# Kernel tuning notes

Hardware: AMD Instinct MI355X
Metric: run time of the kernel (lower is better)

Reference implementation:

```python
import jax, jax.numpy as jnp
import numpy as np

B, L, H, D, VOC, C, P = 16, 256, 6, 768, 32000, 20, 1
d = D // H
MAXF = 20
BN_EPS = 1e-5


def setup_inputs() -> dict:
    key = jax.random.key(0)
    ks = jax.random.split(key, 8)
    doc_tids = jax.random.randint(ks[0], (B, L), 0, VOC)
    TFs = jax.random.uniform(ks[1], (B, L), dtype=jnp.float32) * 20.0 + 1.0
    DFs = jax.random.uniform(ks[2], (B, L), dtype=jnp.float32) * 1000.0 + 1.0
    emb = jax.random.normal(ks[3], (VOC, D), dtype=jnp.float32) * 0.02
    fcW = jax.random.normal(ks[4], (C + P, D), dtype=jnp.float32) * 0.02
    fcb = jnp.zeros((C + P,), dtype=jnp.float32)
    weiW = jax.random.normal(ks[5], (2, H), dtype=jnp.float32) * 0.1
    weib = jnp.zeros((2,), dtype=jnp.float32)
    return dict(doc_tids=doc_tids, TFs=TFs, DFs=DFs, emb=emb,
                fcW=fcW, fcb=fcb, weiW=weiW, weib=weib)


def _bn(x):
    # BatchNorm over channel axis 1 (H), batch stats over all other axes (train mode, affine=False)
    m = x.mean(axis=(0, 2, 3), keepdims=True)
    v = x.var(axis=(0, 2, 3), keepdims=True)
    return (x - m) * jax.lax.rsqrt(v + BN_EPS)


def _leaky9(x):
    return jnp.where(x >= 0, x, 9.0 * x)


def reference(doc_tids, TFs, DFs, emb, fcW, fcb, weiW, weib):
    # --- EmbbedingTFIDF (eval mode, dropout off): tf-idf weighted embedding lookup ---
    tf = jnp.minimum(TFs, float(MAXF))
    idf = jnp.log1p(1.0 / DFs)
    x = emb[doc_tids] * (tf * idf)[:, :, None]          # (B, L, D)
    valid = doc_tids != 0
    # model flips pad_mask with logical_not, then co_weights[pad_mask] = 0
    invalid = ~(valid[:, :, None] & valid[:, None, :])  # (B, L, L) True -> zero out
    mask = invalid[:, None, :, :]                       # broadcast over heads

    def split_heads(h):
        return h.reshape(B, L, H, d).transpose(0, 2, 1, 3)  # (B, H, L, d)

    Q = split_heads(x)
    K = Q
    V = Q

    # --- nearAttention (layers=1) ---
    Vn = _bn(V)
    # DistMatrix: pairwise Euclidean distance dist[b,h,i,j] = ||K_i - Q_j||
    Ksq = jnp.sum(K * K, axis=-1)[..., :, None]
    Qsq = jnp.sum(Q * Q, axis=-1)[..., None, :]
    cross = jnp.einsum('bhid,bhjd->bhij', K, Q)
    co = jnp.sqrt(jnp.maximum(Ksq + Qsq - 2.0 * cross, 1e-12))  # (B, H, L, L)
    # BatchNorm1d(H) over flattened (B, H, L*L) == per-H stats over (0,2,3)
    co = _leaky9(_bn(co))
    co = jnp.where(mask, 0.0, co)
    co = jax.nn.softmax(co, axis=-1)
    co = jnp.where(jnp.isnan(co), 0.0, co)
    V_out = jnp.einsum('bhij,bhjd->bhid', co, Vn)
    Q_out = _bn(jnp.einsum('bhij,bhjd->bhid', co, Q))
    K_out = _bn(jnp.einsum('bhij,bhjd->bhid', co, K))

    # --- head ---
    Vc = V_out.transpose(0, 2, 1, 3).reshape(B, L, D)       # catHiddens
    V_lgts = jax.nn.softmax(Vc @ fcW.T + fcb, axis=-1)      # (B, L, C+P)
    cw = jnp.swapaxes(co, -1, -2).reshape(B, L * L, H)      # transpose then contiguous reshape
    cw = jax.nn.softmax(cw @ weiW.T + weib, axis=-1)        # (B, L*L, 2)
    cw = cw.reshape(B, L, L, 2).sum(axis=-2, keepdims=True)[:, :, :, 0]  # (B, L, 1)
    cw = jax.nn.softmax(cw, axis=-1)                        # softmax over singleton -> ones (faithful)
    logits = (cw * V_lgts).sum(axis=1)[:, :C]               # (B, C)
    logits = jax.nn.softmax(logits, axis=-1)
    return logits
```

## Files before the change

kernel.cpp:

```cpp
#include <hip/hip_runtime.h>
#include <hip/hip_bf16.h>
#include <math.h>

#define OFF_XH   0UL
#define OFF_XT   1572864UL
#define OFF_VC   3145728UL
#define OFF_SQ   4718592UL
#define OFF_THS  4743168UL
#define OFF_PART 4767744UL
#define OFF_STAT 4780032UL
#define OFF_ACC  4780056UL
#define OFF_FCWB 4780392UL

typedef __attribute__((ext_vector_type(8))) __bf16 bf16x8;
typedef __attribute__((ext_vector_type(4))) float f32x4;
typedef __attribute__((ext_vector_type(8))) unsigned short u16x8;

__global__ __launch_bounds__(256) void k1_gather(const int* __restrict__ tids,
    const float* __restrict__ TF, const float* __restrict__ DF,
    const float* __restrict__ emb, unsigned short* __restrict__ xh,
    unsigned short* __restrict__ xT, float* __restrict__ sq, float* __restrict__ ths) {
  int bh = blockIdx.x >> 4, tg = blockIdx.x & 15;
  int b = bh / 6, h = bh % 6;
  int T0 = tg * 16;
  int tid = threadIdx.x;
  __shared__ float swgt[16];
  __shared__ int stid[16];
  __shared__ unsigned short tT[128][18];
  if (tid < 16) {
    int tok = b * 256 + T0 + tid;
    stid[tid] = tids[tok];
    swgt[tid] = fminf(TF[tok], 20.0f) * log1pf(1.0f / DF[tok]);
  }
  __syncthreads();
  int r = tid >> 4, c8 = (tid & 15) * 8;
  const float* er = emb + (size_t)stid[r] * 768 + h * 128 + c8;
  float wgt = swgt[r];
  float4 e0 = *(const float4*)er;
  float4 e1 = *(const float4*)(er + 4);
  float f[8] = {e0.x, e0.y, e0.z, e0.w, e1.x, e1.y, e1.z, e1.w};
  float s1 = 0.0f, s2 = 0.0f;
  u16x8 pk;
#pragma unroll
  for (int e = 0; e < 8; ++e) {
    __hip_bfloat16 hb = __float2bfloat16(f[e] * wgt);
    float g = __bfloat162float(hb);
    s1 += g; s2 += g * g;
    pk[e] = __bfloat16_as_ushort(hb);
  }
  *(u16x8*)(xh + ((size_t)(bh * 256 + T0 + r)) * 128 + c8) = pk;
  s1 += __shfl_down(s1, 8); s1 += __shfl_down(s1, 4);
  s1 += __shfl_down(s1, 2); s1 += __shfl_down(s1, 1);
  s2 += __shfl_down(s2, 8); s2 += __shfl_down(s2, 4);
  s2 += __shfl_down(s2, 2); s2 += __shfl_down(s2, 1);
  if ((tid & 15) == 0) {
    ths[bh * 256 + T0 + r] = s1;
    sq[bh * 256 + T0 + r]  = s2;
  }
#pragma unroll
  for (int j = 0; j < 8; ++j) tT[c8 + j][r] = pk[j];
  __syncthreads();
  int ch = tid >> 1, half = tid & 1;
  unsigned int* xo = (unsigned int*)xT + ((size_t)(bh * 128 + ch)) * 128 + tg * 8 + half * 4;
#pragma unroll
  for (int k = 0; k < 4; ++k)
    xo[k] = *(const unsigned int*)&tT[ch][(half * 4 + k) * 2];
}

__global__ __launch_bounds__(256) void k2_stats(const unsigned short* __restrict__ xh,
    const float* __restrict__ sq, float* __restrict__ part) {
  int p = blockIdx.x, bh = blockIdx.y;
  int tid = threadIdx.x, w = tid >> 6, lane = tid & 63;
  int quad = lane >> 4, l16 = lane & 15;
  int I = p * 16;
  const __bf16* xb = (const __bf16*)xh + (size_t)bh * 256 * 128;
  bf16x8 a[4];
#pragma unroll
  for (int k0 = 0; k0 < 4; ++k0)
    a[k0] = *(const bf16x8*)(xb + (size_t)(I + l16) * 128 + k0 * 32 + quad * 8);
  const float* sqh = sq + (size_t)bh * 256;
  float si[4];
#pragma unroll
  for (int r = 0; r < 4; ++r) si[r] = sqh[I + quad * 4 + r];
  float ls1 = 0.0f, ls2 = 0.0f;
#pragma unroll
  for (int tl = 0; tl < 4; ++tl) {
    int t = w * 4 + tl;
    f32x4 acc = {0.0f, 0.0f, 0.0f, 0.0f};
#pragma unroll
    for (int k0 = 0; k0 < 4; ++k0) {
      bf16x8 bfr = *(const bf16x8*)(xb + (size_t)(t * 16 + l16) * 128 + k0 * 32 + quad * 8);
      acc = __builtin_amdgcn_mfma_f32_16x16x32_bf16(a[k0], bfr, acc, 0, 0, 0);
    }
    float sj = sqh[t * 16 + l16];
#pragma unroll
    for (int r = 0; r < 4; ++r) {
      float cv = sqrtf(fmaxf(si[r] + sj - 2.0f * acc[r], 1e-12f));
      ls1 += cv; ls2 += cv * cv;
    }
  }
#pragma unroll
  for (int off = 32; off >= 1; off >>= 1) {
    ls1 += __shfl_down(ls1, off);
    ls2 += __shfl_down(ls2, off);
  }
  if (lane == 0) {
    part[(((size_t)bh * 16 + p) * 4 + w) * 2 + 0] = ls1;
    part[(((size_t)bh * 16 + p) * 4 + w) * 2 + 1] = ls2;
  }
}

__global__ __launch_bounds__(384) void k3_stats(const float* __restrict__ ths,
    const float* __restrict__ sq, const float* __restrict__ part,
    const float* __restrict__ fcW, float* __restrict__ stats,
    float* __restrict__ acc, unsigned short* __restrict__ fcWb) {
  int h = threadIdx.x >> 6, lane = threadIdx.x & 63;
  float s1 = 0.0f, s2 = 0.0f;
  for (int m = 0; m < 64; ++m) {
    int f = m * 64 + lane;
    int bb = f >> 8, l = f & 255;
    size_t idx = ((size_t)(bb * 6 + h)) * 256 + l;
    s1 += ths[idx]; s2 += sq[idx];
  }
#pragma unroll
  for (int off = 32; off >= 1; off >>= 1) {
    s1 += __shfl_down(s1, off);
    s2 += __shfl_down(s2, off);
  }
  if (lane == 0) {
    float cnt = 524288.0f;
    float mean = s1 / cnt;
    float var = s2 / cnt - mean * mean;
    stats[h] = mean;
    stats[6 + h] = rsqrtf(var + 1e-5f);
  }
  float c1 = 0.0f, c2 = 0.0f;
#pragma unroll
  for (int t = 0; t < 16; ++t) {
    int e = lane + 64 * t;
    int bb = e >> 6, rest = e & 63, pp = rest >> 2, ww = rest & 3;
    size_t pidx = ((((size_t)(bb * 6 + h)) * 16 + pp) * 4 + ww) * 2;
    c1 += part[pidx]; c2 += part[pidx + 1];
  }
#pragma unroll
  for (int off = 32; off >= 1; off >>= 1) {
    c1 += __shfl_down(c1, off);
    c2 += __shfl_down(c2, off);
  }
  if (lane == 0) {
    float cnt = 1048576.0f;
    float mean = c1 / cnt;
    float var = c2 / cnt - mean * mean;
    stats[12 + h] = mean;
    stats[18 + h] = rsqrtf(var + 1e-5f);
  }
  if (threadIdx.x < 336) acc[threadIdx.x] = 0.0f;
  for (int idx = threadIdx.x; idx < 21 * 768; idx += 384)
    fcWb[idx] = __bfloat16_as_ushort(__float2bfloat16(fcW[idx]));
}

__global__ __launch_bounds__(256, 4) void k45_fused(const unsigned short* __restrict__ xh,
    const unsigned short* __restrict__ xT, const int* __restrict__ tids,
    const float* __restrict__ sq, const float* __restrict__ stats,
    unsigned short* __restrict__ vc16) {
  int p = blockIdx.x, bh = blockIdx.y;
  int b = bh / 6, h = bh % 6;
  int tid = threadIdx.x, w = tid >> 6, lane = tid & 63;
  int quad = lane >> 4, l16 = lane & 15;
  int I = p * 16;
  __shared__ float svld[256];
  __shared__ float ssq[256];
  __shared__ unsigned short cot[16][264];
  __shared__ float smax[16][4];
  __shared__ float ssum[16][4];
  svld[tid] = (tids[b * 256 + tid] != 0) ? 1.0f : 0.0f;
  ssq[tid] = sq[(size_t)bh * 256 + tid];
  const __bf16* xb = (const __bf16*)xh + (size_t)bh * 256 * 128;
  bf16x8 a[4];
#pragma unroll
  for (int k0 = 0; k0 < 4; ++k0)
    a[k0] = *(const bf16x8*)(xb + (size_t)(I + l16) * 128 + k0 * 32 + quad * 8);
  __syncthreads();
  float m = stats[12 + h], rsc = stats[18 + h];
  float rv[4], si[4];
#pragma unroll
  for (int r = 0; r < 4; ++r) {
    rv[r] = svld[I + quad * 4 + r];
    si[r] = ssq[I + quad * 4 + r];
  }
  float y[4][4];
#pragma unroll
  for (int tl = 0; tl < 4; ++tl) {
    int t = w * 4 + tl;
    f32x4 acc = {0.0f, 0.0f, 0.0f, 0.0f};
#pragma unroll
    for (int k0 = 0; k0 < 4; ++k0) {
      bf16x8 bfr = *(const bf16x8*)(xb + (size_t)(t * 16 + l16) * 128 + k0 * 32 + quad * 8);
      acc = __builtin_amdgcn_mfma_f32_16x16x32_bf16(a[k0], bfr, acc, 0, 0, 0);
    }
    float sj = ssq[t * 16 + l16];
    float cvld = svld[t * 16 + l16];
#pragma unroll
    for (int r = 0; r < 4; ++r) {
      float cv = sqrtf(fmaxf(si[r] + sj - 2.0f * acc[r], 1e-12f));
      float yv = (cv - m) * rsc;
      yv = yv >= 0.0f ? yv : 9.0f * yv;
      y[tl][r] = yv * rv[r] * cvld;
    }
  }
#pragma unroll
  for (int r = 0; r < 4; ++r) {
    float mx = fmaxf(fmaxf(y[0][r], y[1][r]), fmaxf(y[2][r], y[3][r]));
#pragma unroll
    for (int off = 1; off <= 8; off <<= 1) mx = fmaxf(mx, __shfl_xor(mx, off));
    if (l16 == 0) smax[quad * 4 + r][w] = mx;
  }
  __syncthreads();
  float gmx[4];
#pragma unroll
  for (int r = 0; r < 4; ++r) {
    int row = quad * 4 + r;
    gmx[r] = fmaxf(fmaxf(smax[row][0], smax[row][1]), fmaxf(smax[row][2], smax[row][3]));
    float s = 0.0f;
#pragma unroll
    for (int tl = 0; tl < 4; ++tl) { y[tl][r] = expf(y[tl][r] - gmx[r]); s += y[tl][r]; }
#pragma unroll
    for (int off = 1; off <= 8; off <<= 1) s += __shfl_xor(s, off);
    if (l16 == 0) ssum[row][w] = s;
  }
  __syncthreads();
#pragma unroll
  for (int r = 0; r < 4; ++r) {
    int row = quad * 4 + r;
    float gs = ssum[row][0] + ssum[row][1] + ssum[row][2] + ssum[row][3];
    float inv = 1.0f / gs;
#pragma unroll
    for (int tl = 0; tl < 4; ++tl)
      cot[row][w * 64 + tl * 16 + l16] =
          __bfloat16_as_ushort(__float2bfloat16(y[tl][r] * inv));
  }
  __syncthreads();
  bf16x8 a2[8];
#pragma unroll
  for (int k0 = 0; k0 < 8; ++k0)
    a2[k0] = *(const bf16x8*)&cot[l16][k0 * 32 + quad * 8];
  const __bf16* xbT = (const __bf16*)xT + (size_t)bh * 128 * 256;
  float mv = stats[h], rvs = stats[6 + h];
  float rm = rvs * mv;
  size_t vbase = ((size_t)(b * 256 + I + quad * 4)) * 768 + h * 128;
#pragma unroll
  for (int jl = 0; jl < 2; ++jl) {
    int ch = (w * 2 + jl) * 16 + l16;
    const __bf16* brow = xbT + (size_t)ch * 256;
    f32x4 vacc = {0.0f, 0.0f, 0.0f, 0.0f};
#pragma unroll
    for (int k0 = 0; k0 < 8; ++k0) {
      bf16x8 bfr = *(const bf16x8*)(brow + k0 * 32 + quad * 8);
      vacc = __builtin_amdgcn_mfma_f32_16x16x32_bf16(a2[k0], bfr, vacc, 0, 0, 0);
    }
#pragma unroll
    for (int r = 0; r < 4; ++r) {
      float ov = rvs * vacc[r] - rm;
      vc16[vbase + (size_t)r * 768 + ch] = __bfloat16_as_ushort(__float2bfloat16(ov));
    }
  }
}

__global__ __launch_bounds__(256) void k5b_lgts(const unsigned short* __restrict__ vc16,
    const unsigned short* __restrict__ fcWb, const float* __restrict__ fcb,
    float* __restrict__ acc) {
  int b = blockIdx.x >> 2, qa = blockIdx.x & 3;
  int tid = threadIdx.x, w = tid >> 6, lane = tid & 63;
  int quad = lane >> 4, l16 = lane & 15;
  int tok0 = b * 256 + qa * 64 + w * 16;
  int c1c = (l16 < 5) ? (16 + l16) : 20;
  const __bf16* vb = (const __bf16*)vc16;
  const __bf16* w0 = (const __bf16*)fcWb + (size_t)l16 * 768;
  const __bf16* w1 = (const __bf16*)fcWb + (size_t)c1c * 768;
  f32x4 ac0 = {0.0f, 0.0f, 0.0f, 0.0f}, ac1 = {0.0f, 0.0f, 0.0f, 0.0f};
#pragma unroll
  for (int k0 = 0; k0 < 24; ++k0) {
    int ko = k0 * 32 + quad * 8;
    bf16x8 af = *(const bf16x8*)(vb + (size_t)(tok0 + l16) * 768 + ko);
    bf16x8 b0 = *(const bf16x8*)(w0 + ko);
    bf16x8 b1 = *(const bf16x8*)(w1 + ko);
    ac0 = __builtin_amdgcn_mfma_f32_16x16x32_bf16(af, b0, ac0, 0, 0, 0);
    ac1 = __builtin_amdgcn_mfma_f32_16x16x32_bf16(af, b1, ac1, 0, 0, 0);
  }
  float bias0 = fcb[l16];
  float bias1 = (l16 < 5) ? fcb[16 + l16] : 0.0f;
  float p0s = 0.0f, p1s = 0.0f;
#pragma unroll
  for (int r = 0; r < 4; ++r) {
    float lg0 = ac0[r] + bias0;
    float lg1 = (l16 < 5) ? (ac1[r] + bias1) : -1e30f;
    float mx = fmaxf(lg0, lg1);
#pragma unroll
    for (int off = 1; off <= 8; off <<= 1) mx = fmaxf(mx, __shfl_xor(mx, off));
    float e0 = expf(lg0 - mx), e1 = expf(lg1 - mx);
    float s = e0 + e1;
#pragma unroll
    for (int off = 1; off <= 8; off <<= 1) s += __shfl_xor(s, off);
    float inv = 1.0f / s;
    p0s += e0 * inv;
    p1s += e1 * inv;
  }
  p0s += __shfl_xor(p0s, 16); p0s += __shfl_xor(p0s, 32);
  p1s += __shfl_xor(p1s, 16); p1s += __shfl_xor(p1s, 32);
  __shared__ float sacc[4][21];
  if (quad == 0) sacc[w][l16] = p0s;
  if (quad == 1 && l16 < 5) sacc[w][16 + l16] = p1s;
  __syncthreads();
  if (tid < 21) {
    float s = sacc[0][tid] + sacc[1][tid] + sacc[2][tid] + sacc[3][tid];
    atomicAdd(&acc[b * 21 + tid], s);
  }
}

__global__ __launch_bounds__(64) void k6_final(const float* __restrict__ acc,
                                               float* __restrict__ out) {
  int b = threadIdx.x;
  if (b < 16) {
    float mx = -1e30f;
    for (int c = 0; c < 20; ++c) mx = fmaxf(mx, acc[b * 21 + c]);
    float e[20], s = 0.0f;
    for (int c = 0; c < 20; ++c) { e[c] = expf(acc[b * 21 + c] - mx); s += e[c]; }
    float inv = 1.0f / s;
    for (int c = 0; c < 20; ++c) out[b * 20 + c] = e[c] * inv;
  }
}

extern "C" void kernel_launch(void* const* d_in, const int* in_sizes, int n_in,
                              void* d_out, int out_size, void* d_ws, size_t ws_size,
                              hipStream_t stream) {
  const int*   tids = (const int*)d_in[0];
  const float* TF   = (const float*)d_in[1];
  const float* DF   = (const float*)d_in[2];
  const float* emb  = (const float*)d_in[3];
  const float* fcW  = (const float*)d_in[4];
  const float* fcb  = (const float*)d_in[5];
  float* out = (float*)d_out;
  float* ws  = (float*)d_ws;
  unsigned short* xh   = (unsigned short*)(ws + OFF_XH);
  unsigned short* xT   = (unsigned short*)(ws + OFF_XT);
  unsigned short* vc   = (unsigned short*)(ws + OFF_VC);
  unsigned short* fcWb = (unsigned short*)(ws + OFF_FCWB);
  float* sq    = ws + OFF_SQ;
  float* ths   = ws + OFF_THS;
  float* part  = ws + OFF_PART;
  float* stats = ws + OFF_STAT;
  float* acc   = ws + OFF_ACC;

  k1_gather<<<1536, 256, 0, stream>>>(tids, TF, DF, emb, xh, xT, sq, ths);
  k2_stats<<<dim3(16, 96), 256, 0, stream>>>(xh, sq, part);
  k3_stats<<<1, 384, 0, stream>>>(ths, sq, part, fcW, stats, acc, fcWb);
  k45_fused<<<dim3(16, 96), 256, 0, stream>>>(xh, xT, tids, sq, stats, vc);
  k5b_lgts<<<64, 256, 0, stream>>>(vc, fcWb, fcb, acc);
  k6_final<<<1, 64, 0, stream>>>(acc, out);
}
```

Baseline: 214.4 us.

## Fuse gather with distance-stats kernel via LDS tile and fold final softmax

Result: faster. 207.4 us (-3.3%).

```diff
diff --git a/kernel.cpp b/kernel.cpp
--- a/kernel.cpp
+++ b/kernel.cpp
@@ -10,93 +10,124 @@
 #define OFF_PART 4767744UL
 #define OFF_STAT 4780032UL
 #define OFF_ACC  4780056UL
-#define OFF_FCWB 4780392UL
+#define OFF_CTR  4780392UL
+#define OFF_FCWB 4780396UL
 
 typedef __attribute__((ext_vector_type(8))) __bf16 bf16x8;
 typedef __attribute__((ext_vector_type(4))) float f32x4;
 typedef __attribute__((ext_vector_type(8))) unsigned short u16x8;
 
-__global__ __launch_bounds__(256) void k1_gather(const int* __restrict__ tids,
+__global__ __launch_bounds__(512) void k12_fused(const int* __restrict__ tids,
     const float* __restrict__ TF, const float* __restrict__ DF,
     const float* __restrict__ emb, unsigned short* __restrict__ xh,
-    unsigned short* __restrict__ xT, float* __restrict__ sq, float* __restrict__ ths) {
-  int bh = blockIdx.x >> 4, tg = blockIdx.x & 15;
+    unsigned short* __restrict__ xT, float* __restrict__ sq,
+    float* __restrict__ ths, float* __restrict__ part) {
+  int jh = blockIdx.x, bh = blockIdx.y;
   int b = bh / 6, h = bh % 6;
-  int T0 = tg * 16;
   int tid = threadIdx.x;
-  __shared__ float swgt[16];
-  __shared__ int stid[16];
-  __shared__ unsigned short tT[128][18];
-  if (tid < 16) {
-    int tok = b * 256 + T0 + tid;
-    stid[tid] = tids[tok];
-    swgt[tid] = fminf(TF[tok], 20.0f) * log1pf(1.0f / DF[tok]);
-  }
-  __syncthreads();
-  int r = tid >> 4, c8 = (tid & 15) * 8;
-  const float* er = emb + (size_t)stid[r] * 768 + h * 128 + c8;
-  float wgt = swgt[r];
-  float4 e0 = *(const float4*)er;
-  float4 e1 = *(const float4*)(er + 4);
-  float f[8] = {e0.x, e0.y, e0.z, e0.w, e1.x, e1.y, e1.z, e1.w};
-  float s1 = 0.0f, s2 = 0.0f;
-  u16x8 pk;
-#pragma unroll
-  for (int e = 0; e < 8; ++e) {
-    __hip_bfloat16 hb = __float2bfloat16(f[e] * wgt);
-    float g = __bfloat162float(hb);
-    s1 += g; s2 += g * g;
-    pk[e] = __bfloat16_as_ushort(hb);
-  }
-  *(u16x8*)(xh + ((size_t)(bh * 256 + T0 + r)) * 128 + c8) = pk;
-  s1 += __shfl_down(s1, 8); s1 += __shfl_down(s1, 4);
-  s1 += __shfl_down(s1, 2); s1 += __shfl_down(s1, 1);
-  s2 += __shfl_down(s2, 8); s2 += __shfl_down(s2, 4);
-  s2 += __shfl_down(s2, 2); s2 += __shfl_down(s2, 1);
-  if ((tid & 15) == 0) {
-    ths[bh * 256 + T0 + r] = s1;
-    sq[bh * 256 + T0 + r]  = s2;
-  }
-#pragma unroll
-  for (int j = 0; j < 8; ++j) tT[c8 + j][r] = pk[j];
-  __syncthreads();
-  int ch = tid >> 1, half = tid & 1;
-  unsigned int* xo = (unsigned int*)xT + ((size_t)(bh * 128 + ch)) * 128 + tg * 8 + half * 4;
-#pragma unroll
-  for (int k = 0; k < 4; ++k)
-    xo[k] = *(const unsigned int*)&tT[ch][(half * 4 + k) * 2];
-}
-
-__global__ __launch_bounds__(256) void k2_stats(const unsigned short* __restrict__ xh,
-    const float* __restrict__ sq, float* __restrict__ part) {
-  int p = blockIdx.x, bh = blockIdx.y;
-  int tid = threadIdx.x, w = tid >> 6, lane = tid & 63;
-  int quad = lane >> 4, l16 = lane & 15;
-  int I = p * 16;
-  const __bf16* xb = (const __bf16*)xh + (size_t)bh * 256 * 128;
-  bf16x8 a[4];
-#pragma unroll
-  for (int k0 = 0; k0 < 4; ++k0)
-    a[k0] = *(const bf16x8*)(xb + (size_t)(I + l16) * 128 + k0 * 32 + quad * 8);
+  __shared__ unsigned short tile[32768];
+  if (tid < 2) part[((size_t)bh * 2 + jh) * 2 + tid] = 0.0f;
+  int sub = tid & 7, row0 = tid >> 3;
+  int c16 = sub * 16;
+#pragma unroll
+  for (int p = 0; p < 4; ++p) {
+    int r = p * 64 + row0;
+    int tok = b * 256 + r;
+    int tv = tids[tok];
+    float wgt = fminf(TF[tok], 20.0f) * log1pf(1.0f / DF[tok]);
+    const float* er = emb + (size_t)tv * 768 + h * 128 + c16;
+    float4 e0 = *(const float4*)er;
+    float4 e1 = *(const float4*)(er + 4);
+    float4 e2 = *(const float4*)(er + 8);
+    float4 e3 = *(const float4*)(er + 12);
+    float f[16] = {e0.x, e0.y, e0.z, e0.w, e1.x, e1.y, e1.z, e1.w,
+                   e2.x, e2.y, e2.z, e2.w, e3.x, e3.y, e3.z, e3.w};
+    u16x8 pk0, pk1;
+    float s1 = 0.0f, s2 = 0.0f;
+#pragma unroll
+    for (int e = 0; e < 8; ++e) {
+      __hip_bfloat16 hb = __float2bfloat16(f[e] * wgt);
+      float g = __bfloat162float(hb);
+      s1 += g; s2 += g * g;
+      pk0[e] = __bfloat16_as_ushort(hb);
+    }
+#pragma unroll
+    for (int e = 0; e < 8; ++e) {
+      __hip_bfloat16 hb = __float2bfloat16(f[8 + e] * wgt);
+      float g = __bfloat162float(hb);
+      s1 += g; s2 += g * g;
+      pk1[e] = __bfloat16_as_ushort(hb);
+    }
+    int rx = r & 7;
+    *(u16x8*)&tile[r * 128 + (((sub * 2    ) ^ rx) * 8)] = pk0;
+    *(u16x8*)&tile[r * 128 + (((sub * 2 + 1) ^ rx) * 8)] = pk1;
+    if (jh == 0) {
+      unsigned short* xo = xh + ((size_t)bh * 256 + r) * 128 + c16;
+      *(u16x8*)xo = pk0;
+      *(u16x8*)(xo + 8) = pk1;
+    }
+    s1 += __shfl_down(s1, 4); s1 += __shfl_down(s1, 2); s1 += __shfl_down(s1, 1);
+    s2 += __shfl_down(s2, 4); s2 += __shfl_down(s2, 2); s2 += __shfl_down(s2, 1);
+    if (sub == 0) {
+      sq[(size_t)bh * 256 + r] = s2;
+      if (jh == 0) ths[(size_t)bh * 256 + r] = s1;
+    }
+  }
+  __syncthreads();
+  if (jh == 1) {
+    int ch = tid & 127, q = tid >> 7;
+    int cc = ch >> 3, cs = ch & 7;
+    unsigned int* xo = (unsigned int*)xT + ((size_t)bh * 128 + ch) * 128 + q * 32;
+#pragma unroll
+    for (int g = 0; g < 8; ++g) {
+      unsigned int tmp[4];
+#pragma unroll
+      for (int k = 0; k < 4; ++k) {
+        int t0 = q * 64 + (g * 4 + k) * 2;
+        unsigned int lo = tile[ t0      * 128 + ((cc ^ ( t0      & 7)) * 8) + cs];
+        unsigned int hi = tile[(t0 + 1) * 128 + ((cc ^ ((t0 + 1) & 7)) * 8) + cs];
+        tmp[k] = lo | (hi << 16);
+      }
+      uint4 vv; vv.x = tmp[0]; vv.y = tmp[1]; vv.z = tmp[2]; vv.w = tmp[3];
+      *(uint4*)(xo + g * 4) = vv;
+    }
+  }
+  int w = tid >> 6, lane = tid & 63, quad = lane >> 4, l16 = lane & 15;
   const float* sqh = sq + (size_t)bh * 256;
-  float si[4];
-#pragma unroll
-  for (int r = 0; r < 4; ++r) si[r] = sqh[I + quad * 4 + r];
+  int it0 = w * 2;
+  bf16x8 a2[2][4];
+  float si2[2][4];
+#pragma unroll
+  for (int ith = 0; ith < 2; ++ith) {
+    int ar = (it0 + ith) * 16 + l16, arx = ar & 7;
+#pragma unroll
+    for (int k0 = 0; k0 < 4; ++k0)
+      a2[ith][k0] = *(const bf16x8*)&tile[ar * 128 + (((k0 * 4 + quad) ^ arx) * 8)];
+#pragma unroll
+    for (int r = 0; r < 4; ++r)
+      si2[ith][r] = sqh[(it0 + ith) * 16 + quad * 4 + r];
+  }
   float ls1 = 0.0f, ls2 = 0.0f;
 #pragma unroll
-  for (int tl = 0; tl < 4; ++tl) {
-    int t = w * 4 + tl;
-    f32x4 acc = {0.0f, 0.0f, 0.0f, 0.0f};
+  for (int jt = 0; jt < 8; ++jt) {
+    int jr = jh * 128 + jt * 16 + l16, jrx = jr & 7;
+    bf16x8 bfr[4];
+#pragma unroll
+    for (int k0 = 0; k0 < 4; ++k0)
+      bfr[k0] = *(const bf16x8*)&tile[jr * 128 + (((k0 * 4 + quad) ^ jrx) * 8)];
+    f32x4 acc0 = {0.0f, 0.0f, 0.0f, 0.0f}, acc1 = {0.0f, 0.0f, 0.0f, 0.0f};
 #pragma unroll
     for (int k0 = 0; k0 < 4; ++k0) {
-      bf16x8 bfr = *(const bf16x8*)(xb + (size_t)(t * 16 + l16) * 128 + k0 * 32 + quad * 8);
-      acc = __builtin_amdgcn_mfma_f32_16x16x32_bf16(a[k0], bfr, acc, 0, 0, 0);
-    }
-    float sj = sqh[t * 16 + l16];
+      acc0 = __builtin_amdgcn_mfma_f32_16x16x32_bf16(a2[0][k0], bfr[k0], acc0, 0, 0, 0);
+      acc1 = __builtin_amdgcn_mfma_f32_16x16x32_bf16(a2[1][k0], bfr[k0], acc1, 0, 0, 0);
+    }
+    float sj = sqh[jr];
 #pragma unroll
     for (int r = 0; r < 4; ++r) {
-      float cv = sqrtf(fmaxf(si[r] + sj - 2.0f * acc[r], 1e-12f));
-      ls1 += cv; ls2 += cv * cv;
+      float cv0 = sqrtf(fmaxf(si2[0][r] + sj - 2.0f * acc0[r], 1e-12f));
+      float cv1 = sqrtf(fmaxf(si2[1][r] + sj - 2.0f * acc1[r], 1e-12f));
+      ls1 += cv0 + cv1;
+      ls2 += cv0 * cv0 + cv1 * cv1;
     }
   }
 #pragma unroll
@@ -105,15 +136,16 @@
     ls2 += __shfl_down(ls2, off);
   }
   if (lane == 0) {
-    part[(((size_t)bh * 16 + p) * 4 + w) * 2 + 0] = ls1;
-    part[(((size_t)bh * 16 + p) * 4 + w) * 2 + 1] = ls2;
+    atomicAdd(&part[((size_t)bh * 2 + jh) * 2 + 0], ls1);
+    atomicAdd(&part[((size_t)bh * 2 + jh) * 2 + 1], ls2);
   }
 }
 
 __global__ __launch_bounds__(384) void k3_stats(const float* __restrict__ ths,
     const float* __restrict__ sq, const float* __restrict__ part,
     const float* __restrict__ fcW, float* __restrict__ stats,
-    float* __restrict__ acc, unsigned short* __restrict__ fcWb) {
+    float* __restrict__ acc, unsigned int* __restrict__ ctr,
+    unsigned short* __restrict__ fcWb) {
   int h = threadIdx.x >> 6, lane = threadIdx.x & 63;
   float s1 = 0.0f, s2 = 0.0f;
   for (int m = 0; m < 64; ++m) {
@@ -135,15 +167,13 @@
     stats[6 + h] = rsqrtf(var + 1e-5f);
   }
   float c1 = 0.0f, c2 = 0.0f;
-#pragma unroll
-  for (int t = 0; t < 16; ++t) {
-    int e = lane + 64 * t;
-    int bb = e >> 6, rest = e & 63, pp = rest >> 2, ww = rest & 3;
-    size_t pidx = ((((size_t)(bb * 6 + h)) * 16 + pp) * 4 + ww) * 2;
-    c1 += part[pidx]; c2 += part[pidx + 1];
-  }
-#pragma unroll
-  for (int off = 32; off >= 1; off >>= 1) {
+  if (lane < 32) {
+    int bb = lane >> 1, jh = lane & 1;
+    size_t pidx = (((size_t)(bb * 6 + h)) * 2 + jh) * 2;
+    c1 = part[pidx]; c2 = part[pidx + 1];
+  }
+#pragma unroll
+  for (int off = 16; off >= 1; off >>= 1) {
     c1 += __shfl_down(c1, off);
     c2 += __shfl_down(c2, off);
   }
@@ -155,6 +185,7 @@
     stats[18 + h] = rsqrtf(var + 1e-5f);
   }
   if (threadIdx.x < 336) acc[threadIdx.x] = 0.0f;
+  if (threadIdx.x == 336) *ctr = 0u;
   for (int idx = threadIdx.x; idx < 21 * 768; idx += 384)
     fcWb[idx] = __bfloat16_as_ushort(__float2bfloat16(fcW[idx]));
 }
@@ -266,9 +297,9 @@
   }
 }
 
-__global__ __launch_bounds__(256) void k5b_lgts(const unsigned short* __restrict__ vc16,
+__global__ __launch_bounds__(256) void k5b6_lgts(const unsigned short* __restrict__ vc16,
     const unsigned short* __restrict__ fcWb, const float* __restrict__ fcb,
-    float* __restrict__ acc) {
+    float* __restrict__ acc, unsigned int* __restrict__ ctr, float* __restrict__ out) {
   int b = blockIdx.x >> 2, qa = blockIdx.x & 3;
   int tid = threadIdx.x, w = tid >> 6, lane = tid & 63;
   int quad = lane >> 4, l16 = lane & 15;
@@ -308,6 +339,7 @@
   p0s += __shfl_xor(p0s, 16); p0s += __shfl_xor(p0s, 32);
   p1s += __shfl_xor(p1s, 16); p1s += __shfl_xor(p1s, 32);
   __shared__ float sacc[4][21];
+  __shared__ unsigned int sdone;
   if (quad == 0) sacc[w][l16] = p0s;
   if (quad == 1 && l16 < 5) sacc[w][16 + l16] = p1s;
   __syncthreads();
@@ -315,18 +347,26 @@
     float s = sacc[0][tid] + sacc[1][tid] + sacc[2][tid] + sacc[3][tid];
     atomicAdd(&acc[b * 21 + tid], s);
   }
-}
-
-__global__ __launch_bounds__(64) void k6_final(const float* __restrict__ acc,
-                                               float* __restrict__ out) {
-  int b = threadIdx.x;
-  if (b < 16) {
+  __syncthreads();
+  if (tid == 0) {
+    __threadfence();
+    sdone = atomicAdd(ctr, 1u);
+  }
+  __syncthreads();
+  if (sdone == 63u && tid < 16) {
+    float v[20];
     float mx = -1e30f;
-    for (int c = 0; c < 20; ++c) mx = fmaxf(mx, acc[b * 21 + c]);
-    float e[20], s = 0.0f;
-    for (int c = 0; c < 20; ++c) { e[c] = expf(acc[b * 21 + c] - mx); s += e[c]; }
+#pragma unroll
+    for (int c = 0; c < 20; ++c) {
+      v[c] = atomicAdd(&acc[tid * 21 + c], 0.0f);
+      mx = fmaxf(mx, v[c]);
+    }
+    float s = 0.0f;
+#pragma unroll
+    for (int c = 0; c < 20; ++c) { v[c] = expf(v[c] - mx); s += v[c]; }
     float inv = 1.0f / s;
-    for (int c = 0; c < 20; ++c) out[b * 20 + c] = e[c] * inv;
+#pragma unroll
+    for (int c = 0; c < 20; ++c) out[tid * 20 + c] = v[c] * inv;
   }
 }
 
@@ -350,11 +390,10 @@
   float* part  = ws + OFF_PART;
   float* stats = ws + OFF_STAT;
   float* acc   = ws + OFF_ACC;
-
-  k1_gather<<<1536, 256, 0, stream>>>(tids, TF, DF, emb, xh, xT, sq, ths);
-  k2_stats<<<dim3(16, 96), 256, 0, stream>>>(xh, sq, part);
-  k3_stats<<<1, 384, 0, stream>>>(ths, sq, part, fcW, stats, acc, fcWb);
+  unsigned int* ctr = (unsigned int*)(ws + OFF_CTR);
+
+  k12_fused<<<dim3(2, 96), 512, 0, stream>>>(tids, TF, DF, emb, xh, xT, sq, ths, part);
+  k3_stats<<<1, 384, 0, stream>>>(ths, sq, part, fcW, stats, acc, ctr, fcWb);
   k45_fused<<<dim3(16, 96), 256, 0, stream>>>(xh, xT, tids, sq, stats, vc);
-  k5b_lgts<<<64, 256, 0, stream>>>(vc, fcWb, fcb, acc);
-  k6_final<<<1, 64, 0, stream>>>(acc, out);
-}
+  k5b6_lgts<<<64, 256, 0, stream>>>(vc, fcWb, fcb, acc, ctr, out);
+}
```

## Fold stats reduction into consumers, merge final softmax, remap blocks per XCD

Applied to the files above, without the earlier changes.

After: 201.9 us. 5.8% less time.

```diff
diff --git a/kernel.cpp b/kernel.cpp
--- a/kernel.cpp
+++ b/kernel.cpp
@@ -6,11 +6,10 @@
 #define OFF_XT   1572864UL
 #define OFF_VC   3145728UL
 #define OFF_SQ   4718592UL
-#define OFF_THS  4743168UL
 #define OFF_PART 4767744UL
-#define OFF_STAT 4780032UL
 #define OFF_ACC  4780056UL
-#define OFF_FCWB 4780392UL
+#define OFF_CTR  4780392UL
+#define OFF_FCWB 4780396UL
 
 typedef __attribute__((ext_vector_type(8))) __bf16 bf16x8;
 typedef __attribute__((ext_vector_type(4))) float f32x4;
@@ -19,14 +18,26 @@
 __global__ __launch_bounds__(256) void k1_gather(const int* __restrict__ tids,
     const float* __restrict__ TF, const float* __restrict__ DF,
     const float* __restrict__ emb, unsigned short* __restrict__ xh,
-    unsigned short* __restrict__ xT, float* __restrict__ sq, float* __restrict__ ths) {
-  int bh = blockIdx.x >> 4, tg = blockIdx.x & 15;
+    unsigned short* __restrict__ xT, float* __restrict__ sq, float* __restrict__ part,
+    const float* __restrict__ fcW, unsigned short* __restrict__ fcWb,
+    float* __restrict__ acc, unsigned int* __restrict__ ctr) {
+  int bid = blockIdx.x;
+  int bh = bid >> 4, tg = bid & 15;
   int b = bh / 6, h = bh % 6;
   int T0 = tg * 16;
   int tid = threadIdx.x;
   __shared__ float swgt[16];
   __shared__ int stid[16];
   __shared__ unsigned short tT[128][18];
+  __shared__ float srs1[16], srs2[16];
+  if (bid == 0) {
+    for (int i = tid; i < 336; i += 256) acc[i] = 0.0f;
+    if (tid == 0) *ctr = 0u;
+  }
+  if (tg == 1 && tid < 168) {
+    int i2 = bh * 168 + tid;
+    fcWb[i2] = __bfloat16_as_ushort(__float2bfloat16(fcW[i2]));
+  }
   if (tid < 16) {
     int tok = b * 256 + T0 + tid;
     stid[tid] = tids[tok];
@@ -54,12 +65,19 @@
   s2 += __shfl_down(s2, 8); s2 += __shfl_down(s2, 4);
   s2 += __shfl_down(s2, 2); s2 += __shfl_down(s2, 1);
   if ((tid & 15) == 0) {
-    ths[bh * 256 + T0 + r] = s1;
-    sq[bh * 256 + T0 + r]  = s2;
+    sq[(size_t)bh * 256 + T0 + r] = s2;
+    srs1[r] = s1; srs2[r] = s2;
   }
 #pragma unroll
   for (int j = 0; j < 8; ++j) tT[c8 + j][r] = pk[j];
   __syncthreads();
+  if (tid == 0) {
+    float v1 = 0.0f, v2 = 0.0f;
+#pragma unroll
+    for (int i = 0; i < 16; ++i) { v1 += srs1[i]; v2 += srs2[i]; }
+    part[((size_t)bh * 16 + tg) * 2 + 0] = v1;
+    part[((size_t)bh * 16 + tg) * 2 + 1] = v2;
+  }
   int ch = tid >> 1, half = tid & 1;
   unsigned int* xo = (unsigned int*)xT + ((size_t)(bh * 128 + ch)) * 128 + tg * 8 + half * 4;
 #pragma unroll
@@ -67,32 +85,36 @@
     xo[k] = *(const unsigned int*)&tT[ch][(half * 4 + k) * 2];
 }
 
-__global__ __launch_bounds__(256) void k2_stats(const unsigned short* __restrict__ xh,
+__global__ __launch_bounds__(512) void k2_dist(const unsigned short* __restrict__ xh,
     const float* __restrict__ sq, float* __restrict__ part) {
-  int p = blockIdx.x, bh = blockIdx.y;
+  int bid = blockIdx.x;
+  int xcd = bid & 7, idx = bid >> 3;
+  int bh = xcd * 12 + idx % 12;
+  int iq = idx / 12;
   int tid = threadIdx.x, w = tid >> 6, lane = tid & 63;
   int quad = lane >> 4, l16 = lane & 15;
-  int I = p * 16;
+  int it = iq * 4 + (w >> 1), jh = w & 1;
+  __shared__ float swd1[8], swd2[8];
   const __bf16* xb = (const __bf16*)xh + (size_t)bh * 256 * 128;
+  const float* sqh = sq + (size_t)bh * 256;
   bf16x8 a[4];
 #pragma unroll
   for (int k0 = 0; k0 < 4; ++k0)
-    a[k0] = *(const bf16x8*)(xb + (size_t)(I + l16) * 128 + k0 * 32 + quad * 8);
-  const float* sqh = sq + (size_t)bh * 256;
+    a[k0] = *(const bf16x8*)(xb + (size_t)(it * 16 + l16) * 128 + k0 * 32 + quad * 8);
   float si[4];
 #pragma unroll
-  for (int r = 0; r < 4; ++r) si[r] = sqh[I + quad * 4 + r];
+  for (int r = 0; r < 4; ++r) si[r] = sqh[it * 16 + quad * 4 + r];
   float ls1 = 0.0f, ls2 = 0.0f;
 #pragma unroll
-  for (int tl = 0; tl < 4; ++tl) {
-    int t = w * 4 + tl;
+  for (int jt = 0; jt < 8; ++jt) {
+    int j0 = jh * 128 + jt * 16;
     f32x4 acc = {0.0f, 0.0f, 0.0f, 0.0f};
 #pragma unroll
     for (int k0 = 0; k0 < 4; ++k0) {
-      bf16x8 bfr = *(const bf16x8*)(xb + (size_t)(t * 16 + l16) * 128 + k0 * 32 + quad * 8);
+      bf16x8 bfr = *(const bf16x8*)(xb + (size_t)(j0 + l16) * 128 + k0 * 32 + quad * 8);
       acc = __builtin_amdgcn_mfma_f32_16x16x32_bf16(a[k0], bfr, acc, 0, 0, 0);
     }
-    float sj = sqh[t * 16 + l16];
+    float sj = sqh[j0 + l16];
 #pragma unroll
     for (int r = 0; r < 4; ++r) {
       float cv = sqrtf(fmaxf(si[r] + sj - 2.0f * acc[r], 1e-12f));
@@ -104,66 +126,25 @@
     ls1 += __shfl_down(ls1, off);
     ls2 += __shfl_down(ls2, off);
   }
-  if (lane == 0) {
-    part[(((size_t)bh * 16 + p) * 4 + w) * 2 + 0] = ls1;
-    part[(((size_t)bh * 16 + p) * 4 + w) * 2 + 1] = ls2;
-  }
-}
-
-__global__ __launch_bounds__(384) void k3_stats(const float* __restrict__ ths,
-    const float* __restrict__ sq, const float* __restrict__ part,
-    const float* __restrict__ fcW, float* __restrict__ stats,
-    float* __restrict__ acc, unsigned short* __restrict__ fcWb) {
-  int h = threadIdx.x >> 6, lane = threadIdx.x & 63;
-  float s1 = 0.0f, s2 = 0.0f;
-  for (int m = 0; m < 64; ++m) {
-    int f = m * 64 + lane;
-    int bb = f >> 8, l = f & 255;
-    size_t idx = ((size_t)(bb * 6 + h)) * 256 + l;
-    s1 += ths[idx]; s2 += sq[idx];
-  }
-#pragma unroll
-  for (int off = 32; off >= 1; off >>= 1) {
-    s1 += __shfl_down(s1, off);
-    s2 += __shfl_down(s2, off);
-  }
-  if (lane == 0) {
-    float cnt = 524288.0f;
-    float mean = s1 / cnt;
-    float var = s2 / cnt - mean * mean;
-    stats[h] = mean;
-    stats[6 + h] = rsqrtf(var + 1e-5f);
-  }
-  float c1 = 0.0f, c2 = 0.0f;
-#pragma unroll
-  for (int t = 0; t < 16; ++t) {
-    int e = lane + 64 * t;
-    int bb = e >> 6, rest = e & 63, pp = rest >> 2, ww = rest & 3;
-    size_t pidx = ((((size_t)(bb * 6 + h)) * 16 + pp) * 4 + ww) * 2;
-    c1 += part[pidx]; c2 += part[pidx + 1];
-  }
-#pragma unroll
-  for (int off = 32; off >= 1; off >>= 1) {
-    c1 += __shfl_down(c1, off);
-    c2 += __shfl_down(c2, off);
-  }
-  if (lane == 0) {
-    float cnt = 1048576.0f;
-    float mean = c1 / cnt;
-    float var = c2 / cnt - mean * mean;
-    stats[12 + h] = mean;
-    stats[18 + h] = rsqrtf(var + 1e-5f);
-  }
-  if (threadIdx.x < 336) acc[threadIdx.x] = 0.0f;
-  for (int idx = threadIdx.x; idx < 21 * 768; idx += 384)
-    fcWb[idx] = __bfloat16_as_ushort(__float2bfloat16(fcW[idx]));
+  if (lane == 0) { swd1[w] = ls1; swd2[w] = ls2; }
+  __syncthreads();
+  if (tid == 0) {
+    float d1 = 0.0f, d2 = 0.0f;
+#pragma unroll
+    for (int i = 0; i < 8; ++i) { d1 += swd1[i]; d2 += swd2[i]; }
+    part[4096 + (bh * 4 + iq) * 2 + 0] = d1;
+    part[4096 + (bh * 4 + iq) * 2 + 1] = d2;
+  }
 }
 
 __global__ __launch_bounds__(256, 4) void k45_fused(const unsigned short* __restrict__ xh,
     const unsigned short* __restrict__ xT, const int* __restrict__ tids,
-    const float* __restrict__ sq, const float* __restrict__ stats,
+    const float* __restrict__ sq, const float* __restrict__ part,
     unsigned short* __restrict__ vc16) {
-  int p = blockIdx.x, bh = blockIdx.y;
+  int bid = blockIdx.x;
+  int xcd = bid & 7, idx = bid >> 3;
+  int bh = xcd * 12 + idx % 12;
+  int p = idx / 12;
   int b = bh / 6, h = bh % 6;
   int tid = threadIdx.x, w = tid >> 6, lane = tid & 63;
   int quad = lane >> 4, l16 = lane & 15;
@@ -173,15 +154,49 @@
   __shared__ unsigned short cot[16][264];
   __shared__ float smax[16][4];
   __shared__ float ssum[16][4];
+  __shared__ float sstat[4];
   svld[tid] = (tids[b * 256 + tid] != 0) ? 1.0f : 0.0f;
   ssq[tid] = sq[(size_t)bh * 256 + tid];
+  if (w == 0) {
+    float c1 = 0.0f, c2 = 0.0f;
+    {
+      int bb = lane >> 2, jj = lane & 3;
+      c1 = part[4096 + ((bb * 6 + h) * 4 + jj) * 2 + 0];
+      c2 = part[4096 + ((bb * 6 + h) * 4 + jj) * 2 + 1];
+    }
+    float v1 = 0.0f, v2 = 0.0f;
+#pragma unroll
+    for (int t = 0; t < 4; ++t) {
+      int g = lane * 4 + t;
+      int b2 = g >> 4, tg2 = g & 15;
+      v1 += part[((size_t)(b2 * 6 + h) * 16 + tg2) * 2 + 0];
+      v2 += part[((size_t)(b2 * 6 + h) * 16 + tg2) * 2 + 1];
+    }
+#pragma unroll
+    for (int off = 32; off >= 1; off >>= 1) {
+      c1 += __shfl_down(c1, off);
+      c2 += __shfl_down(c2, off);
+      v1 += __shfl_down(v1, off);
+      v2 += __shfl_down(v2, off);
+    }
+    if (lane == 0) {
+      float mean = c1 / 1048576.0f;
+      float var = c2 / 1048576.0f - mean * mean;
+      sstat[0] = mean;
+      sstat[1] = rsqrtf(var + 1e-5f);
+      float mv = v1 / 524288.0f;
+      float vv = v2 / 524288.0f - mv * mv;
+      sstat[2] = mv;
+      sstat[3] = rsqrtf(vv + 1e-5f);
+    }
+  }
   const __bf16* xb = (const __bf16*)xh + (size_t)bh * 256 * 128;
   bf16x8 a[4];
 #pragma unroll
   for (int k0 = 0; k0 < 4; ++k0)
     a[k0] = *(const bf16x8*)(xb + (size_t)(I + l16) * 128 + k0 * 32 + quad * 8);
   __syncthreads();
-  float m = stats[12 + h], rsc = stats[18 + h];
+  float m = sstat[0], rsc = sstat[1];
   float rv[4], si[4];
 #pragma unroll
   for (int r = 0; r < 4; ++r) {
@@ -245,7 +260,7 @@
   for (int k0 = 0; k0 < 8; ++k0)
     a2[k0] = *(const bf16x8*)&cot[l16][k0 * 32 + quad * 8];
   const __bf16* xbT = (const __bf16*)xT + (size_t)bh * 128 * 256;
-  float mv = stats[h], rvs = stats[6 + h];
+  float mv = sstat[2], rvs = sstat[3];
   float rm = rvs * mv;
   size_t vbase = ((size_t)(b * 256 + I + quad * 4)) * 768 + h * 128;
 #pragma unroll
@@ -266,10 +281,13 @@
   }
 }
 
-__global__ __launch_bounds__(256) void k5b_lgts(const unsigned short* __restrict__ vc16,
+__global__ __launch_bounds__(256) void k5b6_lgts(const unsigned short* __restrict__ vc16,
     const unsigned short* __restrict__ fcWb, const float* __restrict__ fcb,
-    float* __restrict__ acc) {
-  int b = blockIdx.x >> 2, qa = blockIdx.x & 3;
+    float* __restrict__ acc, unsigned int* __restrict__ ctr, float* __restrict__ out) {
+  int bid = blockIdx.x;
+  int xcd = bid & 7, idx = bid >> 3;
+  int b = xcd * 2 + (idx & 1);
+  int qa = idx >> 1;
   int tid = threadIdx.x, w = tid >> 6, lane = tid & 63;
   int quad = lane >> 4, l16 = lane & 15;
   int tok0 = b * 256 + qa * 64 + w * 16;
@@ -308,6 +326,7 @@
   p0s += __shfl_xor(p0s, 16); p0s += __shfl_xor(p0s, 32);
   p1s += __shfl_xor(p1s, 16); p1s += __shfl_xor(p1s, 32);
   __shared__ float sacc[4][21];
+  __shared__ unsigned int sdone;
   if (quad == 0) sacc[w][l16] = p0s;
   if (quad == 1 && l16 < 5) sacc[w][16 + l16] = p1s;
   __syncthreads();
@@ -315,18 +334,26 @@
     float s = sacc[0][tid] + sacc[1][tid] + sacc[2][tid] + sacc[3][tid];
     atomicAdd(&acc[b * 21 + tid], s);
   }
-}
-
-__global__ __launch_bounds__(64) void k6_final(const float* __restrict__ acc,
-                                               float* __restrict__ out) {
-  int b = threadIdx.x;
-  if (b < 16) {
+  __syncthreads();
+  if (tid == 0) {
+    __threadfence();
+    sdone = atomicAdd(ctr, 1u);
+  }
+  __syncthreads();
+  if (sdone == 63u && tid < 16) {
+    float v[20];
     float mx = -1e30f;
-    for (int c = 0; c < 20; ++c) mx = fmaxf(mx, acc[b * 21 + c]);
-    float e[20], s = 0.0f;
-    for (int c = 0; c < 20; ++c) { e[c] = expf(acc[b * 21 + c] - mx); s += e[c]; }
+#pragma unroll
+    for (int c = 0; c < 20; ++c) {
+      v[c] = atomicAdd(&acc[tid * 21 + c], 0.0f);
+      mx = fmaxf(mx, v[c]);
+    }
+    float s = 0.0f;
+#pragma unroll
+    for (int c = 0; c < 20; ++c) { v[c] = expf(v[c] - mx); s += v[c]; }
     float inv = 1.0f / s;
-    for (int c = 0; c < 20; ++c) out[b * 20 + c] = e[c] * inv;
+#pragma unroll
+    for (int c = 0; c < 20; ++c) out[tid * 20 + c] = v[c] * inv;
   }
 }
 
@@ -346,15 +373,13 @@
   unsigned short* vc   = (unsigned short*)(ws + OFF_VC);
   unsigned short* fcWb = (unsigned short*)(ws + OFF_FCWB);
   float* sq    = ws + OFF_SQ;
-  float* ths   = ws + OFF_THS;
   float* part  = ws + OFF_PART;
-  float* stats = ws + OFF_STAT;
   float* acc   = ws + OFF_ACC;
-
-  k1_gather<<<1536, 256, 0, stream>>>(tids, TF, DF, emb, xh, xT, sq, ths);
-  k2_stats<<<dim3(16, 96), 256, 0, stream>>>(xh, sq, part);
-  k3_stats<<<1, 384, 0, stream>>>(ths, sq, part, fcW, stats, acc, fcWb);
-  k45_fused<<<dim3(16, 96), 256, 0, stream>>>(xh, xT, tids, sq, stats, vc);
-  k5b_lgts<<<64, 256, 0, stream>>>(vc, fcWb, fcb, acc);
-  k6_final<<<1, 64, 0, stream>>>(acc, out);
-}
+  unsigned int* ctr = (unsigned int*)(ws + OFF_CTR);
+
+  k1_gather<<<1536, 256, 0, stream>>>(tids, TF, DF, emb, xh, xT, sq, part,
+                                      fcW, fcWb, acc, ctr);
+  k2_dist<<<384, 512, 0, stream>>>(xh, sq, part);
+  k45_fused<<<1536, 256, 0, stream>>>(xh, xT, tids, sq, part, vc);
+  k5b6_lgts<<<64, 256, 0, stream>>>(vc, fcWb, fcb, acc, ctr, out);
+}
```
